# Kernel optimization log

Hardware: AMD Instinct MI355X
Metric: run time of the kernel (lower is better)

Reference implementation:

```python
import jax, jax.numpy as jnp
import numpy as np

E, F, H = 8, 4096, 2048  # num_experts, ffn_hidden_size, hidden_size
B, S, K = 2, 1024, 4     # batch, seq_len, top_k


def setup_inputs() -> dict:
    key = jax.random.key(0)
    ks = jax.random.split(key, 7)
    x = jax.random.normal(ks[0], (B, S, H), dtype=jnp.float32)
    weights = jax.random.uniform(ks[1], (B * S, E), dtype=jnp.float32)
    top_weights = jax.random.uniform(ks[2], (B * S, K), dtype=jnp.float32)
    top_experts = jax.random.randint(ks[3], (B * S, K), 0, E)
    w1 = jax.random.normal(ks[4], (E, F, H), dtype=jnp.float32) * 0.02
    v1 = jax.random.normal(ks[5], (E, F, H), dtype=jnp.float32) * 0.02
    w2 = jax.random.normal(ks[6], (E, F, H), dtype=jnp.float32) * 0.02
    return {"x": x, "weights": weights, "top_weights": top_weights,
            "top_experts": top_experts, "w1": w1, "v1": v1, "w2": w2}


def reference(x, weights, top_weights, top_experts, w1, v1, w2):
    # weights (router probs) is accepted but unused, matching the torch forward.
    bsz, q_len, hidden = x.shape
    xt = x.reshape(-1, hidden)  # [T, H]
    num_experts = w1.shape[0]
    # scale[t, e] = sum_k top_weights[t, k] * (top_experts[t, k] == e)
    onehot = jax.nn.one_hot(top_experts, num_experts, dtype=xt.dtype)  # [T, K, E]
    scale = jnp.einsum("tke,tk->te", onehot, top_weights)  # [T, E]
    out = jnp.zeros_like(xt)
    for e in range(num_experts):  # fixed small expert loop, dense+masked combine
        gate = xt @ w1[e].T          # [T, F]
        up = xt @ v1[e].T            # [T, F]
        h = jax.nn.silu(gate) * up   # DbrxExpertGLU
        out = out + (h @ w2[e]) * scale[:, e:e + 1]
    return out.reshape(bsz, q_len, hidden)
```

## Files before the change

kernel.cpp:

```cpp
#include <hip/hip_runtime.h>
#include <hip/hip_bf16.h>

#define NE 8
#define FF 4096
#define HH 2048
#define TT 2048
#define KTOP 4

typedef unsigned short u16;
typedef unsigned int u32;
typedef __attribute__((ext_vector_type(8))) short bf16x8;
typedef __attribute__((ext_vector_type(4))) float f32x4;

#define CFENCE asm volatile("" ::: "memory")

__device__ __forceinline__ u16 f2u(float f) {
  __hip_bfloat16 b = __float2bfloat16(f);
  return *reinterpret_cast<u16*>(&b);
}
__device__ __forceinline__ float u2f(u16 u) {
  union { u32 i; float f; } c; c.i = ((u32)u) << 16; return c.f;
}

__device__ __forceinline__ void gld16(void* lds, const void* g) {
  __builtin_amdgcn_global_load_lds(
      (const __attribute__((address_space(1))) void*)g,
      (__attribute__((address_space(3))) void*)lds, 16, 0, 0);
}

__global__ void k_build(const int* __restrict__ te, int* __restrict__ cnt,
                        int* __restrict__ tok, int* __restrict__ posmap) {
  const int e = blockIdx.x;
  const int tl = threadIdx.x;
  const int base = tl * 8;
  int mem[8];
  int my = 0;
  #pragma unroll
  for (int i = 0; i < 8; ++i) {
    const int t = base + i;
    bool m = false;
    #pragma unroll
    for (int k = 0; k < KTOP; ++k) m |= (te[t * KTOP + k] == e);
    mem[i] = m ? 1 : 0;
    my += mem[i];
  }
  __shared__ int s[256];
  s[tl] = my;
  __syncthreads();
  for (int off = 1; off < 256; off <<= 1) {
    int v = (tl >= off) ? s[tl - off] : 0;
    __syncthreads();
    s[tl] += v;
    __syncthreads();
  }
  int r = s[tl] - my;
  if (tl == 255) cnt[e] = s[255];
  #pragma unroll
  for (int i = 0; i < 8; ++i) {
    if (mem[i]) {
      const int t = base + i;
      tok[e * TT + r] = t;
      posmap[t * NE + e] = r;
      ++r;
    }
  }
}

__global__ void k_cast4(const float4* __restrict__ src, ushort4* __restrict__ dst, int n4) {
  int stride = gridDim.x * blockDim.x;
  for (int i = blockIdx.x * blockDim.x + threadIdx.x; i < n4; i += stride) {
    float4 f = src[i];
    ushort4 o;
    o.x = f2u(f.x); o.y = f2u(f.y); o.z = f2u(f.z); o.w = f2u(f.w);
    dst[i] = o;
  }
}

template<int MODE>
__global__ __launch_bounds__(512)
void gemm256(const u16* __restrict__ Aall, const u16* __restrict__ Ball,
             const int* __restrict__ cnt, void* __restrict__ Oall,
             const float* __restrict__ W1, const float* __restrict__ V1,
             const int* __restrict__ tok, const u16* __restrict__ Zp,
             const float* __restrict__ W2, u16* __restrict__ W2t) {
  constexpr int KD  = (MODE == 0) ? HH : FF;
  constexpr int NTK = KD / 64;
  constexpr int NT  = (MODE == 0) ? 32 : 8;
  constexpr int NB  = (MODE == 0) ? 2 * FF : HH;
  constexpr int NWG = (MODE == 0) ? 2048 : 512;

  __shared__ __align__(16) u16 smem[65536];
  const int bid = blockIdx.x;
  const int tid = threadIdx.x;

  if (MODE == 0 && bid >= NWG) {
    float (*tile)[65] = reinterpret_cast<float(*)[65]>(smem);
    const int r = tid >> 3;
    const int c0 = (tid & 7) * 8;
    for (int i = 0; i < 8; ++i) {
      const int g = (bid - NWG) * 8 + i;
      const int e = g >> 11;
      const int rem = g & 2047;
      const int f0 = (rem >> 5) << 6;
      const int h0 = (rem & 31) << 6;
      const float* src = W2 + (size_t)e * FF * HH + (size_t)(f0 + r) * HH + h0 + c0;
      float4 a = ((const float4*)src)[0];
      float4 b = ((const float4*)src)[1];
      tile[r][c0 + 0] = a.x; tile[r][c0 + 1] = a.y;
      tile[r][c0 + 2] = a.z; tile[r][c0 + 3] = a.w;
      tile[r][c0 + 4] = b.x; tile[r][c0 + 5] = b.y;
      tile[r][c0 + 6] = b.z; tile[r][c0 + 7] = b.w;
      __syncthreads();
      union { ushort u[8]; bf16x8 v; } o;
      #pragma unroll
      for (int j = 0; j < 8; ++j) o.u[j] = f2u(tile[c0 + j][r]);
      *(bf16x8*)(W2t + (size_t)e * HH * FF + (size_t)(h0 + r) * FF + f0 + c0) = o.v;
      __syncthreads();
    }
    return;
  }

  const int swz = (bid & 7) * (NWG >> 3) + (bid >> 3);
  const int e   = swz / (8 * NT);
  const int rem = swz % (8 * NT);
  const int ntl = rem / 8;
  const int mt  = rem % 8;
  const int c = cnt[e];
  const int mcap = (c + 255) & ~255;
  if (mt * 256 >= mcap) return;

  const int lane = tid & 63;
  const int wave = tid >> 6;
  const int wm = wave >> 2;
  const int wn = wave & 3;

  const bool skipW = (wm == 1) && (mt * 256 + 128 >= c);

  const int tq = tid >> 2;
  const int tc = (((tid & 3) ^ ((tid >> 3) & 3)) << 3);

  const u16* pA0;
  const u16* pA1;
  if constexpr (MODE == 0) {
    const int r0 = mt * 256 + tq;
    const int r1 = r0 + 128;
    pA0 = ((r0 < c) ? Aall + (size_t)tok[e * TT + r0] * HH : Zp) + tc;
    pA1 = ((r1 < c) ? Aall + (size_t)tok[e * TT + r1] * HH : Zp) + tc;
  } else {
    const u16* A = Aall + (size_t)e * TT * KD + (size_t)(mt * 256) * KD;
    pA0 = A + (size_t)tq * KD + tc;
    pA1 = pA0 + (size_t)128 * KD;
  }

  auto stageA = [&](int d, int ks, int kt) {
    u16* dst = smem + ((d * 2 + ks) << 13) + tid * 8;
    const int off = kt * 64 + ks * 32;
    gld16(dst,        pA0 + off);
    gld16(dst + 4096, pA1 + off);
  };

  const u16* pB = Ball + (size_t)e * NB * KD + (size_t)(ntl * 256) * KD
                       + (size_t)tq * KD + tc;
  auto stageB = [&](int d, int ks, int kt) {
    u16* dst = smem + 32768 + ((d * 2 + ks) << 13) + tid * 8;
    const u16* src = pB + kt * 64 + ks * 32;
    gld16(dst,        src);
    gld16(dst + 4096, src + (size_t)128 * KD);
  };

  const float* pW = nullptr;
  if constexpr (MODE == 0) {
    const int sel = (tq >> 4) & 1;
    const int fr  = ntl * 128 + (tq >> 5) * 16 + (tq & 15);
    pW = (sel ? V1 : W1) + ((size_t)(e * FF + fr)) * HH + (tid & 3) * 8;
  }
  float4 br0[4], br1[4];
  auto issueB = [&](float4* br, int ks, int kt) {
    const float* s = pW + kt * 64 + ks * 32;
    br[0] = ((const float4*)s)[0];
    br[1] = ((const float4*)s)[1];
    const float* s2 = s + (size_t)64 * HH;
    br[2] = ((const float4*)s2)[0];
    br[3] = ((const float4*)s2)[1];
  };
  auto cvtB = [&](float4* br, int d, int ks) {
    u16* dst = smem + 32768 + ((d * 2 + ks) << 13) + tq * 32 + tc;
    union { ushort u[8]; bf16x8 v; } lo, hi;
    lo.u[0]=f2u(br[0].x); lo.u[1]=f2u(br[0].y); lo.u[2]=f2u(br[0].z); lo.u[3]=f2u(br[0].w);
    lo.u[4]=f2u(br[1].x); lo.u[5]=f2u(br[1].y); lo.u[6]=f2u(br[1].z); lo.u[7]=f2u(br[1].w);
    hi.u[0]=f2u(br[2].x); hi.u[1]=f2u(br[2].y); hi.u[2]=f2u(br[2].z); hi.u[3]=f2u(br[2].w);
    hi.u[4]=f2u(br[3].x); hi.u[5]=f2u(br[3].y); hi.u[6]=f2u(br[3].z); hi.u[7]=f2u(br[3].w);
    *(bf16x8*)(dst)        = lo.v;
    *(bf16x8*)(dst + 4096) = hi.v;
  };

  f32x4 acc[8][4];
  #pragma unroll
  for (int m = 0; m < 8; ++m)
    #pragma unroll
    for (int n = 0; n < 4; ++n)
      acc[m][n] = (f32x4){0.f, 0.f, 0.f, 0.f};

  const int lr = lane & 15;
  const int lc = ((((lane >> 4) & 3) ^ ((lane >> 1) & 3)) << 3);

  bf16x8 af[4], bf[4];
  auto rdA = [&](int d, int ks, int mq) {
    const u16* blk = smem + ((d * 2 + ks) << 13);
    #pragma unroll
    for (int m = 0; m < 4; ++m)
      af[m] = *(const bf16x8*)(blk + (wm * 128 + mq * 64 + m * 16 + lr) * 32 + lc);
  };
  auto rdB = [&](int d, int ks) {
    const u16* blk = smem + 32768 + ((d * 2 + ks) << 13);
    #pragma unroll
    for (int n = 0; n < 4; ++n)
      bf[n] = *(const bf16x8*)(blk + (wn * 64 + n * 16 + lr) * 32 + lc);
  };
  auto vmwait = [&](int n) {
    switch (n) {
      case 0:  asm volatile("s_waitcnt vmcnt(0)"  ::: "memory"); break;
      case 6:  asm volatile("s_waitcnt vmcnt(6)"  ::: "memory"); break;
      default: asm volatile("s_waitcnt vmcnt(8)"  ::: "memory"); break;
    }
  };
  auto MF = [&](int mq) {
    __builtin_amdgcn_s_setprio(1);
    #pragma unroll
    for (int m = 0; m < 4; ++m)
      #pragma unroll
      for (int n = 0; n < 4; ++n)
        acc[mq * 4 + m][n] = __builtin_amdgcn_mfma_f32_16x16x32_bf16(
            af[m], bf[n], acc[mq * 4 + m][n], 0, 0, 0);
    __builtin_amdgcn_s_setprio(0);
  };

  if constexpr (MODE == 0) {
    issueB(br0, 0, 0);
    issueB(br1, 1, 0);
    stageA(0, 0, 0);
    stageA(0, 1, 0);
    cvtB(br0, 0, 0);
    cvtB(br1, 0, 1);
    issueB(br0, 0, 1);
    issueB(br1, 1, 1);
    vmwait(8);
    asm volatile("s_waitcnt lgkmcnt(0)" ::: "memory");
  } else {
    stageA(0, 0, 0); stageA(0, 1, 0);
    stageB(0, 0, 0); stageB(0, 1, 0);
    vmwait(0);
  }
  __builtin_amdgcn_s_barrier();
  CFENCE;

  for (int t = 0; t < NTK; ++t) {
    const int d = t & 1, dn = d ^ 1;
    const bool hasN  = (t + 1 < NTK);
    const bool hasN2 = (t + 2 < NTK);

    if (!skipW) { rdB(d, 0); rdA(d, 0, 0); }
    if (hasN) {
      stageA(dn, 0, t + 1);
      stageA(dn, 1, t + 1);
      if constexpr (MODE == 1) { stageB(dn, 0, t + 1); stageB(dn, 1, t + 1); }
    }
    __builtin_amdgcn_sched_barrier(0);
    if (!skipW) {
      MF(0);
      rdA(d, 0, 1);
      MF(1);
    }
    if constexpr (MODE == 0) {
      if (hasN)  cvtB(br0, dn, 0);
      if (hasN2) issueB(br0, 0, t + 2);
    }
    if (!skipW) {
      rdB(d, 1); rdA(d, 1, 0);
      MF(0);
    }
    if constexpr (MODE == 0) {
      if (hasN)  cvtB(br1, dn, 1);
      if (hasN2) issueB(br1, 1, t + 2);
    }
    if (!skipW) {
      rdA(d, 1, 1);
      MF(1);
    }
    if constexpr (MODE == 0) {
      asm volatile("s_waitcnt lgkmcnt(0)" ::: "memory");
      vmwait(hasN2 ? 8 : 0);
    } else {
      vmwait(0);
    }
    __builtin_amdgcn_s_barrier();
    CFENCE;
  }

  if (skipW) return;

  const int rb = mt * 256 + wm * 128 + ((lane >> 4) << 2);
  if (MODE == 0) {
    u16* H = (u16*)Oall + (size_t)e * TT * FF;
    const int fb = ntl * 128 + wn * 32 + lr;
    #pragma unroll
    for (int m = 0; m < 8; ++m)
      #pragma unroll
      for (int np = 0; np < 2; ++np)
        #pragma unroll
        for (int j = 0; j < 4; ++j) {
          float g = acc[m][2*np][j];
          float u = acc[m][2*np + 1][j];
          float hh = (g / (1.f + __expf(-g))) * u;
          H[(size_t)(rb + m*16 + j) * FF + fb + np*16] = f2u(hh);
        }
  } else {
    u16* D = (u16*)Oall + (size_t)e * TT * HH;
    const int cb = ntl * 256 + wn * 64 + lr;
    #pragma unroll
    for (int m = 0; m < 8; ++m)
      #pragma unroll
      for (int n = 0; n < 4; ++n)
        #pragma unroll
        for (int j = 0; j < 4; ++j)
          D[(size_t)(rb + m*16 + j) * HH + cb + n*16] = f2u(acc[m][n][j]);
  }
}

__global__ void k_combine(const float* __restrict__ tw, const int* __restrict__ te,
                          const int* __restrict__ posmap, const u16* __restrict__ dcomp,
                          float* __restrict__ out) {
  const int t = blockIdx.x;
  const int c0 = threadIdx.x * 8;
  float a[8] = {0.f, 0.f, 0.f, 0.f, 0.f, 0.f, 0.f, 0.f};
  #pragma unroll
  for (int k = 0; k < KTOP; ++k) {
    const int e = te[t * KTOP + k];
    const float w = tw[t * KTOP + k];
    const int r = posmap[t * NE + e];
    const u16* row = dcomp + ((size_t)e * TT + r) * HH + c0;
    union { bf16x8 v; ushort u[8]; } x;
    x.v = *(const bf16x8*)row;
    #pragma unroll
    for (int j = 0; j < 8; ++j) a[j] += w * u2f(x.u[j]);
  }
  float* o = out + (size_t)t * HH + c0;
  ((float4*)o)[0] = (float4){a[0], a[1], a[2], a[3]};
  ((float4*)o)[1] = (float4){a[4], a[5], a[6], a[7]};
}

extern "C" void kernel_launch(void* const* d_in, const int* in_sizes, int n_in,
                              void* d_out, int out_size, void* d_ws, size_t ws_size,
                              hipStream_t stream) {
  const float* x  = (const float*)d_in[0];
  const float* tw = (const float*)d_in[2];
  const int*   te = (const int*)d_in[3];
  const float* w1 = (const float*)d_in[4];
  const float* v1 = (const float*)d_in[5];
  const float* w2 = (const float*)d_in[6];
  float* out = (float*)d_out;

  char* p = (char*)d_ws;
  int*   cnt    = (int*)p;   p += 256;
  int*   tok    = (int*)p;   p += (size_t)NE * TT * 4;
  int*   posmap = (int*)p;   p += (size_t)TT * NE * 4;
  u16*   zp     = (u16*)p;   p += (size_t)HH * 2;
  u16*   xb     = (u16*)p;   p += (size_t)TT * HH * 2;
  u16*   w2tb   = (u16*)p;   p += (size_t)NE * HH * FF * 2;
  u16*   hc     = (u16*)p;   p += (size_t)NE * TT * FF * 2;
  u16*   dcomp  = (u16*)p;   p += (size_t)NE * TT * HH * 2;

  hipMemsetAsync(zp, 0, (size_t)HH * 2, stream);
  k_build<<<NE, 256, 0, stream>>>(te, cnt, tok, posmap);
  k_cast4<<<1024, 256, 0, stream>>>((const float4*)x, (ushort4*)xb, TT * HH / 4);

  gemm256<0><<<4096, 512, 0, stream>>>(xb, nullptr, cnt, hc, w1, v1, tok, zp,
                                       w2, w2tb);
  gemm256<1><<<512, 512, 0, stream>>>(hc, w2tb, cnt, dcomp, nullptr, nullptr,
                                      nullptr, nullptr, nullptr, nullptr);
  k_combine<<<TT, 256, 0, stream>>>(tw, te, posmap, dcomp, out);
}
```

Baseline: 488.1 us.

## Halve workgroup to 4 waves with 128x128 per-wave tiles in grouped GEMM

Both GEMM modes now run 256 threads per block instead of 512. Each wave covers a 128x128 output tile (8x8 MFMA accumulators) instead of 128x64, and each thread issues twice as many global-to-LDS loads. The goal is more MFMA work per LDS fragment read and fewer waves contending for LDS. The cost is a much higher VGPR load (256 accumulator floats per thread) and less latency hiding per CU. The W2 transpose side path is adjusted to cover its tile with the smaller block.

```diff
diff --git a/kernel.cpp b/kernel.cpp
--- a/kernel.cpp
+++ b/kernel.cpp
@@ -77,7 +77,7 @@
 }
 
 template<int MODE>
-__global__ __launch_bounds__(512)
+__global__ __launch_bounds__(256)
 void gemm256(const u16* __restrict__ Aall, const u16* __restrict__ Ball,
              const int* __restrict__ cnt, void* __restrict__ Oall,
              const float* __restrict__ W1, const float* __restrict__ V1,
@@ -95,8 +95,8 @@
 
   if (MODE == 0 && bid >= NWG) {
     float (*tile)[65] = reinterpret_cast<float(*)[65]>(smem);
-    const int r = tid >> 3;
-    const int c0 = (tid & 7) * 8;
+    const int r  = tid >> 2;
+    const int c0 = (tid & 3) * 16;
     for (int i = 0; i < 8; ++i) {
       const int g = (bid - NWG) * 8 + i;
       const int e = g >> 11;
@@ -104,17 +104,21 @@
       const int f0 = (rem >> 5) << 6;
       const int h0 = (rem & 31) << 6;
       const float* src = W2 + (size_t)e * FF * HH + (size_t)(f0 + r) * HH + h0 + c0;
-      float4 a = ((const float4*)src)[0];
-      float4 b = ((const float4*)src)[1];
-      tile[r][c0 + 0] = a.x; tile[r][c0 + 1] = a.y;
-      tile[r][c0 + 2] = a.z; tile[r][c0 + 3] = a.w;
-      tile[r][c0 + 4] = b.x; tile[r][c0 + 5] = b.y;
-      tile[r][c0 + 6] = b.z; tile[r][c0 + 7] = b.w;
+      #pragma unroll
+      for (int q = 0; q < 4; ++q) {
+        float4 a = ((const float4*)src)[q];
+        tile[r][c0 + q*4 + 0] = a.x; tile[r][c0 + q*4 + 1] = a.y;
+        tile[r][c0 + q*4 + 2] = a.z; tile[r][c0 + q*4 + 3] = a.w;
+      }
       __syncthreads();
-      union { ushort u[8]; bf16x8 v; } o;
-      #pragma unroll
-      for (int j = 0; j < 8; ++j) o.u[j] = f2u(tile[c0 + j][r]);
-      *(bf16x8*)(W2t + (size_t)e * HH * FF + (size_t)(h0 + r) * FF + f0 + c0) = o.v;
+      union { ushort u[8]; bf16x8 v; } o1, o2;
+      #pragma unroll
+      for (int j = 0; j < 8; ++j) o1.u[j] = f2u(tile[c0 + j][r]);
+      #pragma unroll
+      for (int j = 0; j < 8; ++j) o2.u[j] = f2u(tile[c0 + 8 + j][r]);
+      u16* dst = W2t + (size_t)e * HH * FF + (size_t)(h0 + r) * FF + f0 + c0;
+      *(bf16x8*)dst       = o1.v;
+      *(bf16x8*)(dst + 8) = o2.v;
       __syncthreads();
     }
     return;
@@ -131,32 +135,34 @@
 
   const int lane = tid & 63;
   const int wave = tid >> 6;
-  const int wm = wave >> 2;
-  const int wn = wave & 3;
+  const int wm = wave >> 1;
+  const int wn = wave & 1;
 
   const bool skipW = (wm == 1) && (mt * 256 + 128 >= c);
 
   const int tq = tid >> 2;
   const int tc = (((tid & 3) ^ ((tid >> 3) & 3)) << 3);
 
-  const u16* pA0;
-  const u16* pA1;
+  const u16* pA[4];
   if constexpr (MODE == 0) {
-    const int r0 = mt * 256 + tq;
-    const int r1 = r0 + 128;
-    pA0 = ((r0 < c) ? Aall + (size_t)tok[e * TT + r0] * HH : Zp) + tc;
-    pA1 = ((r1 < c) ? Aall + (size_t)tok[e * TT + r1] * HH : Zp) + tc;
+    #pragma unroll
+    for (int i = 0; i < 4; ++i) {
+      const int r = mt * 256 + tq + 64 * i;
+      pA[i] = ((r < c) ? Aall + (size_t)tok[e * TT + r] * HH : Zp) + tc;
+    }
   } else {
     const u16* A = Aall + (size_t)e * TT * KD + (size_t)(mt * 256) * KD;
-    pA0 = A + (size_t)tq * KD + tc;
-    pA1 = pA0 + (size_t)128 * KD;
+    #pragma unroll
+    for (int i = 0; i < 4; ++i)
+      pA[i] = A + (size_t)(tq + 64 * i) * KD + tc;
   }
 
   auto stageA = [&](int d, int ks, int kt) {
     u16* dst = smem + ((d * 2 + ks) << 13) + tid * 8;
     const int off = kt * 64 + ks * 32;
-    gld16(dst,        pA0 + off);
-    gld16(dst + 4096, pA1 + off);
+    #pragma unroll
+    for (int i = 0; i < 4; ++i)
+      gld16(dst + i * 2048, pA[i] + off);
   };
 
   const u16* pB = Ball + (size_t)e * NB * KD + (size_t)(ntl * 256) * KD
@@ -164,74 +170,76 @@
   auto stageB = [&](int d, int ks, int kt) {
     u16* dst = smem + 32768 + ((d * 2 + ks) << 13) + tid * 8;
     const u16* src = pB + kt * 64 + ks * 32;
-    gld16(dst,        src);
-    gld16(dst + 4096, src + (size_t)128 * KD);
+    #pragma unroll
+    for (int i = 0; i < 4; ++i)
+      gld16(dst + i * 2048, src + (size_t)(64 * i) * KD);
   };
 
   const float* pW = nullptr;
   if constexpr (MODE == 0) {
     const int sel = (tq >> 4) & 1;
-    const int fr  = ntl * 128 + (tq >> 5) * 16 + (tq & 15);
-    pW = (sel ? V1 : W1) + ((size_t)(e * FF + fr)) * HH + (tid & 3) * 8;
-  }
-  float4 br0[4], br1[4];
+    const int fr0 = ntl * 128 + (tq >> 5) * 16 + (tq & 15);
+    pW = (sel ? V1 : W1) + ((size_t)(e * FF + fr0)) * HH + (tid & 3) * 8;
+  }
+  float4 br0[8], br1[8];
   auto issueB = [&](float4* br, int ks, int kt) {
-    const float* s = pW + kt * 64 + ks * 32;
-    br[0] = ((const float4*)s)[0];
-    br[1] = ((const float4*)s)[1];
-    const float* s2 = s + (size_t)64 * HH;
-    br[2] = ((const float4*)s2)[0];
-    br[3] = ((const float4*)s2)[1];
+    #pragma unroll
+    for (int i = 0; i < 4; ++i) {
+      const float* s = pW + (size_t)(32 * i) * HH + kt * 64 + ks * 32;
+      br[2*i]   = ((const float4*)s)[0];
+      br[2*i+1] = ((const float4*)s)[1];
+    }
   };
   auto cvtB = [&](float4* br, int d, int ks) {
     u16* dst = smem + 32768 + ((d * 2 + ks) << 13) + tq * 32 + tc;
-    union { ushort u[8]; bf16x8 v; } lo, hi;
-    lo.u[0]=f2u(br[0].x); lo.u[1]=f2u(br[0].y); lo.u[2]=f2u(br[0].z); lo.u[3]=f2u(br[0].w);
-    lo.u[4]=f2u(br[1].x); lo.u[5]=f2u(br[1].y); lo.u[6]=f2u(br[1].z); lo.u[7]=f2u(br[1].w);
-    hi.u[0]=f2u(br[2].x); hi.u[1]=f2u(br[2].y); hi.u[2]=f2u(br[2].z); hi.u[3]=f2u(br[2].w);
-    hi.u[4]=f2u(br[3].x); hi.u[5]=f2u(br[3].y); hi.u[6]=f2u(br[3].z); hi.u[7]=f2u(br[3].w);
-    *(bf16x8*)(dst)        = lo.v;
-    *(bf16x8*)(dst + 4096) = hi.v;
-  };
-
-  f32x4 acc[8][4];
+    #pragma unroll
+    for (int i = 0; i < 4; ++i) {
+      union { ushort u[8]; bf16x8 v; } o;
+      o.u[0]=f2u(br[2*i].x); o.u[1]=f2u(br[2*i].y);
+      o.u[2]=f2u(br[2*i].z); o.u[3]=f2u(br[2*i].w);
+      o.u[4]=f2u(br[2*i+1].x); o.u[5]=f2u(br[2*i+1].y);
+      o.u[6]=f2u(br[2*i+1].z); o.u[7]=f2u(br[2*i+1].w);
+      *(bf16x8*)(dst + i * 2048) = o.v;
+    }
+  };
+
+  f32x4 acc[8][8];
   #pragma unroll
   for (int m = 0; m < 8; ++m)
     #pragma unroll
-    for (int n = 0; n < 4; ++n)
+    for (int n = 0; n < 8; ++n)
       acc[m][n] = (f32x4){0.f, 0.f, 0.f, 0.f};
 
   const int lr = lane & 15;
   const int lc = ((((lane >> 4) & 3) ^ ((lane >> 1) & 3)) << 3);
 
-  bf16x8 af[4], bf[4];
-  auto rdA = [&](int d, int ks, int mq) {
+  bf16x8 af[8], bf[8];
+  auto rdA = [&](int d, int ks) {
     const u16* blk = smem + ((d * 2 + ks) << 13);
     #pragma unroll
-    for (int m = 0; m < 4; ++m)
-      af[m] = *(const bf16x8*)(blk + (wm * 128 + mq * 64 + m * 16 + lr) * 32 + lc);
+    for (int m = 0; m < 8; ++m)
+      af[m] = *(const bf16x8*)(blk + (wm * 128 + m * 16 + lr) * 32 + lc);
   };
   auto rdB = [&](int d, int ks) {
     const u16* blk = smem + 32768 + ((d * 2 + ks) << 13);
     #pragma unroll
-    for (int n = 0; n < 4; ++n)
-      bf[n] = *(const bf16x8*)(blk + (wn * 64 + n * 16 + lr) * 32 + lc);
+    for (int n = 0; n < 8; ++n)
+      bf[n] = *(const bf16x8*)(blk + (wn * 128 + n * 16 + lr) * 32 + lc);
   };
   auto vmwait = [&](int n) {
     switch (n) {
       case 0:  asm volatile("s_waitcnt vmcnt(0)"  ::: "memory"); break;
-      case 6:  asm volatile("s_waitcnt vmcnt(6)"  ::: "memory"); break;
-      default: asm volatile("s_waitcnt vmcnt(8)"  ::: "memory"); break;
-    }
-  };
-  auto MF = [&](int mq) {
+      default: asm volatile("s_waitcnt vmcnt(16)" ::: "memory"); break;
+    }
+  };
+  auto MF = [&]() {
     __builtin_amdgcn_s_setprio(1);
     #pragma unroll
-    for (int m = 0; m < 4; ++m)
-      #pragma unroll
-      for (int n = 0; n < 4; ++n)
-        acc[mq * 4 + m][n] = __builtin_amdgcn_mfma_f32_16x16x32_bf16(
-            af[m], bf[n], acc[mq * 4 + m][n], 0, 0, 0);
+    for (int m = 0; m < 8; ++m)
+      #pragma unroll
+      for (int n = 0; n < 8; ++n)
+        acc[m][n] = __builtin_amdgcn_mfma_f32_16x16x32_bf16(
+            af[m], bf[n], acc[m][n], 0, 0, 0);
     __builtin_amdgcn_s_setprio(0);
   };
 
@@ -244,7 +252,7 @@
     cvtB(br1, 0, 1);
     issueB(br0, 0, 1);
     issueB(br1, 1, 1);
-    vmwait(8);
+    vmwait(16);
     asm volatile("s_waitcnt lgkmcnt(0)" ::: "memory");
   } else {
     stageA(0, 0, 0); stageA(0, 1, 0);
@@ -259,37 +267,26 @@
     const bool hasN  = (t + 1 < NTK);
     const bool hasN2 = (t + 2 < NTK);
 
-    if (!skipW) { rdB(d, 0); rdA(d, 0, 0); }
+    if (!skipW) { rdB(d, 0); rdA(d, 0); }
     if (hasN) {
       stageA(dn, 0, t + 1);
       stageA(dn, 1, t + 1);
       if constexpr (MODE == 1) { stageB(dn, 0, t + 1); stageB(dn, 1, t + 1); }
     }
     __builtin_amdgcn_sched_barrier(0);
-    if (!skipW) {
-      MF(0);
-      rdA(d, 0, 1);
-      MF(1);
-    }
+    if (!skipW) MF();
     if constexpr (MODE == 0) {
       if (hasN)  cvtB(br0, dn, 0);
       if (hasN2) issueB(br0, 0, t + 2);
     }
-    if (!skipW) {
-      rdB(d, 1); rdA(d, 1, 0);
-      MF(0);
-    }
+    if (!skipW) { rdB(d, 1); rdA(d, 1); MF(); }
     if constexpr (MODE == 0) {
       if (hasN)  cvtB(br1, dn, 1);
       if (hasN2) issueB(br1, 1, t + 2);
     }
-    if (!skipW) {
-      rdA(d, 1, 1);
-      MF(1);
-    }
     if constexpr (MODE == 0) {
       asm volatile("s_waitcnt lgkmcnt(0)" ::: "memory");
-      vmwait(hasN2 ? 8 : 0);
+      vmwait(hasN2 ? 16 : 0);
     } else {
       vmwait(0);
     }
@@ -302,11 +299,11 @@
   const int rb = mt * 256 + wm * 128 + ((lane >> 4) << 2);
   if (MODE == 0) {
     u16* H = (u16*)Oall + (size_t)e * TT * FF;
-    const int fb = ntl * 128 + wn * 32 + lr;
+    const int fb = ntl * 128 + wn * 64 + lr;
     #pragma unroll
     for (int m = 0; m < 8; ++m)
       #pragma unroll
-      for (int np = 0; np < 2; ++np)
+      for (int np = 0; np < 4; ++np)
         #pragma unroll
         for (int j = 0; j < 4; ++j) {
           float g = acc[m][2*np][j];
@@ -316,11 +313,11 @@
         }
   } else {
     u16* D = (u16*)Oall + (size_t)e * TT * HH;
-    const int cb = ntl * 256 + wn * 64 + lr;
+    const int cb = ntl * 256 + wn * 128 + lr;
     #pragma unroll
     for (int m = 0; m < 8; ++m)
       #pragma unroll
-      for (int n = 0; n < 4; ++n)
+      for (int n = 0; n < 8; ++n)
         #pragma unroll
         for (int j = 0; j < 4; ++j)
           D[(size_t)(rb + m*16 + j) * HH + cb + n*16] = f2u(acc[m][n][j]);
@@ -374,9 +371,9 @@
   k_build<<<NE, 256, 0, stream>>>(te, cnt, tok, posmap);
   k_cast4<<<1024, 256, 0, stream>>>((const float4*)x, (ushort4*)xb, TT * HH / 4);
 
-  gemm256<0><<<4096, 512, 0, stream>>>(xb, nullptr, cnt, hc, w1, v1, tok, zp,
+  gemm256<0><<<4096, 256, 0, stream>>>(xb, nullptr, cnt, hc, w1, v1, tok, zp,
                                        w2, w2tb);
-  gemm256<1><<<512, 512, 0, stream>>>(hc, w2tb, cnt, dcomp, nullptr, nullptr,
+  gemm256<1><<<512, 256, 0, stream>>>(hc, w2tb, cnt, dcomp, nullptr, nullptr,
                                       nullptr, nullptr, nullptr, nullptr);
   k_combine<<<TT, 256, 0, stream>>>(tw, te, posmap, dcomp, out);
 }
```

Result: slower. 572.2 us (+17.2%).
